# Kernel tuning notes

Hardware: AMD Instinct MI355X
Metric: run time of the kernel (lower is better)

Reference implementation:

```python
import jax, jax.numpy as jnp
import numpy as np

HID = 8
PRED_LEN = 12
SCALE = 4.4


def lstm_cell(x, h, c, Wih, Whh, bih, bhh):
    # torch.nn.LSTMCell gate order: i, f, g, o
    gates = x @ Wih.T + h @ Whh.T + (bih + bhh)  # (B, 4*HID)
    i, f, g, o = jnp.split(gates, 4, axis=-1)
    i = jax.nn.sigmoid(i)
    f = jax.nn.sigmoid(f)
    g = jnp.tanh(g)
    o = jax.nn.sigmoid(o)
    c_new = f * c + i * g
    h_new = o * jnp.tanh(c_new)
    return h_new, c_new


def setup_inputs() -> dict:
    key = jax.random.key(0)
    ks = jax.random.split(key, 12)
    B = 1048576
    obs_traj = jax.random.normal(ks[0], (8, B, 2), dtype=jnp.float32)
    h0 = jax.random.normal(ks[1], (B, HID), dtype=jnp.float32)
    c0 = jax.random.normal(ks[2], (B, HID), dtype=jnp.float32)
    s = 0.1
    Wih_t = jax.random.normal(ks[3], (4 * HID, 2), dtype=jnp.float32) * s
    Whh_t = jax.random.normal(ks[4], (4 * HID, HID), dtype=jnp.float32) * s
    bih_t = jax.random.normal(ks[5], (4 * HID,), dtype=jnp.float32) * s
    bhh_t = jax.random.normal(ks[6], (4 * HID,), dtype=jnp.float32) * s
    Wih_p = jax.random.normal(ks[7], (4 * HID, 2), dtype=jnp.float32) * s
    Whh_p = jax.random.normal(ks[8], (4 * HID, HID), dtype=jnp.float32) * s
    bih_p = jax.random.normal(ks[9], (4 * HID,), dtype=jnp.float32) * s
    bhh_p = jax.random.normal(ks[10], (4 * HID,), dtype=jnp.float32) * s
    Wp = jax.random.normal(ks[11], (2, HID), dtype=jnp.float32) * s
    bp = jnp.zeros((2,), dtype=jnp.float32)
    return {"obs_traj": obs_traj, "h0": h0, "c0": c0,
            "Wih_t": Wih_t, "Whh_t": Whh_t, "bih_t": bih_t, "bhh_t": bhh_t,
            "Wih_p": Wih_p, "Whh_p": Whh_p, "bih_p": bih_p, "bhh_p": bhh_p,
            "Wp": Wp, "bp": bp}


def reference(obs_traj, h0, c0, Wih_t, Whh_t, bih_t, bhh_t,
              Wih_p, Whh_p, bih_p, bhh_p, Wp, bp):
    B = obs_traj.shape[1]

    # --- encoder: scan over obs_len steps ---
    def enc_step(carry, x_t):
        h, c = carry
        x = jax.nn.relu(x_t)  # F.relu(input_t)
        h, c = lstm_cell(x, h, c, Wih_t, Whh_t, bih_t, bhh_t)
        return (h, c), None

    (h_enc, _), _ = jax.lax.scan(enc_step, (h0, c0), obs_traj)

    h_dec = h_enc
    c_dec = jnp.zeros_like(h_enc)
    out0 = jnp.zeros((B, 2), dtype=obs_traj.dtype)

    def dec_step(carry, _):
        h, c, out = carry
        x = jax.lax.stop_gradient(out)  # output.detach()
        h, c = lstm_cell(x, h, c, Wih_p, Whh_p, bih_p, bhh_p)
        out = jnp.tanh(h @ Wp.T + bp) * SCALE
        return (h, c, out), out

    _, pred_traj = jax.lax.scan(dec_step, (h_dec, c_dec, out0), None, length=PRED_LEN)
    return pred_traj  # (PRED_LEN, B, 2)
```

## Files before the change

kernel.cpp:

```cpp
#include <hip/hip_runtime.h>

#define HID 8
#define OBS_LEN 8
#define PRED_LEN 12
#define SCALE 4.4f
#define BLOCK 256
#define ELEMS_PER_BLOCK 128

#define LOG2E 1.44269504f
#define ECLAMP 16.0f

typedef __attribute__((ext_vector_type(8)))  _Float16 half8;
typedef __attribute__((ext_vector_type(2)))  _Float16 half2v;
typedef __attribute__((ext_vector_type(16))) float    f32x16;
typedef __attribute__((ext_vector_type(2)))  float    v2f;

union H8 { half8 v; half2v p[4]; };
struct AB { half8 hi, lo; };
struct H2 { _Float16 hi, lo; };

__device__ __forceinline__ v2f splat(float v) { v2f r; r.x = v; r.y = v; return r; }

__device__ __forceinline__ v2f vfma(v2f a, v2f b, v2f c) {
    return __builtin_elementwise_fma(a, b, c);
}

__device__ __forceinline__ v2f exp2v(v2f a) {
    v2f r;
    r.x = __builtin_amdgcn_exp2f(a.x);
    r.y = __builtin_amdgcn_exp2f(a.y);
    return r;
}

__device__ __forceinline__ half2v pkrtz(float a, float b) {
    return __builtin_bit_cast(half2v, __builtin_amdgcn_cvt_pkrtz(a, b));
}

__device__ __forceinline__ H2 split1(float v) {
    H2 r;
    r.hi = (_Float16)v;
    r.lo = (_Float16)(v - (float)r.hi);
    return r;
}

__device__ __forceinline__ void split_pair_v(v2f ab, half2v& hi, half2v& lo) {
    hi = pkrtz(ab.x, ab.y);
    v2f hc; hc.x = (float)hi.x; hc.y = (float)hi.y;
    const v2f res = ab - hc;
    lo = pkrtz(res.x, res.y);
}

__device__ __forceinline__ void quad_inv(const v2f d[2], v2f inv[2]) {
    const v2f p2 = d[0] * d[1];
    const float r = __builtin_amdgcn_rcpf(p2.x * p2.y);
    const v2f t = splat(r) * p2;
    v2f ts; ts.x = t.y; ts.y = t.x;
    inv[0] = ts * d[1];
    inv[1] = ts * d[0];
}

__device__ __forceinline__ AB build_A(int m, int half_,
    const float* __restrict__ Wih, const float* __restrict__ Whh,
    const float* __restrict__ bih, const float* __restrict__ bhh)
{
    const float k = ((m >> 3) == 2) ? (-2.0f * LOG2E) : (-LOG2E);
    float w[8];
    if (half_ == 0) {
        w[0] = Wih[m * 2 + 0] * k;
        w[1] = Wih[m * 2 + 1] * k;
        w[2] = Whh[m * 8 + 0] * k;
        w[3] = Whh[m * 8 + 1] * k;
        w[4] = Whh[m * 8 + 2] * k;
        w[5] = Whh[m * 8 + 3] * k;
        w[6] = (bih[m] + bhh[m]) * k;
        w[7] = 0.0f;
    } else {
        w[0] = 0.0f;
        w[1] = 0.0f;
        w[2] = Whh[m * 8 + 4] * k;
        w[3] = Whh[m * 8 + 5] * k;
        w[4] = Whh[m * 8 + 6] * k;
        w[5] = Whh[m * 8 + 7] * k;
        w[6] = 0.0f;
        w[7] = 0.0f;
    }
    AB r;
#pragma unroll
    for (int i = 0; i < 8; ++i) {
        const H2 s = split1(w[i]);
        r.hi[i] = s.hi;
        r.lo[i] = s.lo;
    }
    return r;
}

__device__ __forceinline__ AB build_B(v2f x01, const v2f h[2]) {
    H8 hi, lo;
    split_pair_v(x01, hi.p[0], lo.p[0]);
    split_pair_v(h[0], hi.p[1], lo.p[1]);
    split_pair_v(h[1], hi.p[2], lo.p[2]);
    const half2v one0 = {(_Float16)1.0f, (_Float16)0.0f};
    const half2v zz   = {(_Float16)0.0f, (_Float16)0.0f};
    hi.p[3] = one0;
    lo.p[3] = zz;
    AB r; r.hi = hi.v; r.lo = lo.v;
    return r;
}

__device__ __forceinline__ void lstm_pointwise(const f32x16& acc, v2f c[2], v2f h[2]) {
    const v2f vone = splat(1.0f);
    v2f num1[2], den1[2], uo[2];
#pragma unroll
    for (int p = 0; p < 2; ++p) {
        v2f ai, af, ag, ao;
        ai.x = acc[2 * p + 0];  ai.y = acc[2 * p + 1];
        af.x = acc[4 + 2 * p];  af.y = acc[5 + 2 * p];
        ag.x = acc[8 + 2 * p];  ag.y = acc[9 + 2 * p];
        ao.x = acc[12 + 2 * p]; ao.y = acc[13 + 2 * p];
        const v2f ei = exp2v(ai);
        const v2f ef = exp2v(af);
        const v2f eg = exp2v(ag);
        const v2f eo = exp2v(ao);
        const v2f uf = ef + vone;
        const v2f vg = eg + vone;
        const v2f tg = vone - eg;
        const v2f uiv = vfma(ei, vg, vg);
        num1[p] = vfma(tg, uf, c[p] * uiv);
        den1[p] = uf * uiv;
        uo[p] = eo + vone;
    }
    v2f inv1[2];
    quad_inv(den1, inv1);

    v2f den2[2], ecs[2];
#pragma unroll
    for (int p = 0; p < 2; ++p) {
        const v2f cn = num1[p] * inv1[p];
        c[p] = cn;
        const v2f s0 = cn * splat(-2.0f * LOG2E);
        v2f s; s.x = fminf(s0.x, ECLAMP); s.y = fminf(s0.y, ECLAMP);
        const v2f ec = exp2v(s);
        den2[p] = vfma(ec, uo[p], uo[p]);
        ecs[p] = ec;
    }
    v2f inv2[2];
    quad_inv(den2, inv2);
    h[0] = vfma(-ecs[0], inv2[0], inv2[0]);
    h[1] = vfma(-ecs[1], inv2[1], inv2[1]);
}

__device__ __forceinline__ void lstm_mfma_step(const AB& A, const AB& B, const f32x16& Z,
                                               v2f c[2], v2f h[2]) {
    f32x16 acc = __builtin_amdgcn_mfma_f32_32x32x16_f16(A.hi, B.hi, Z, 0, 0, 0);
    acc = __builtin_amdgcn_mfma_f32_32x32x16_f16(A.hi, B.lo, acc, 0, 0, 0);
    acc = __builtin_amdgcn_mfma_f32_32x32x16_f16(A.lo, B.hi, acc, 0, 0, 0);
    lstm_pointwise(acc, c, h);
}

__global__ __launch_bounds__(BLOCK) void MYLSTM_88201448390683_kernel(
    const float* __restrict__ obs,
    const float* __restrict__ h0,
    const float* __restrict__ c0,
    const float* __restrict__ Wih_t, const float* __restrict__ Whh_t,
    const float* __restrict__ bih_t, const float* __restrict__ bhh_t,
    const float* __restrict__ Wih_p, const float* __restrict__ Whh_p,
    const float* __restrict__ bih_p, const float* __restrict__ bhh_p,
    const float* __restrict__ Wp,
    const float* __restrict__ bp,
    float* __restrict__ out,
    int B)
{
    const int lane = threadIdx.x & 63;
    const int wid  = threadIdx.x >> 6;
    const int e    = lane & 31;
    const int half = lane >> 5;

    int eg = blockIdx.x * ELEMS_PER_BLOCK + wid * 32 + e;
    const bool ok = eg < B;
    if (!ok) eg = 0;

    const f32x16 kZero = {};

    v2f h[2], c[2];
    {
        const float4 hv = *reinterpret_cast<const float4*>(h0 + (size_t)eg * HID + half * 4);
        const float4 cv = *reinterpret_cast<const float4*>(c0 + (size_t)eg * HID + half * 4);
        h[0].x = hv.x; h[0].y = hv.y; h[1].x = hv.z; h[1].y = hv.w;
        c[0].x = cv.x; c[0].y = cv.y; c[1].x = cv.z; c[1].y = cv.w;
    }

    {
        const AB Aenc = build_A(e, half, Wih_t, Whh_t, bih_t, bhh_t);
        const float* op = obs + (size_t)eg * 2;
        const size_t ostride = (size_t)B * 2;
#pragma unroll 1
        for (int t = 0; t < OBS_LEN; ++t) {
            const v2f xv = *reinterpret_cast<const v2f*>(op);
            op += ostride;
            v2f xr; xr.x = fmaxf(xv.x, 0.0f); xr.y = fmaxf(xv.y, 0.0f);
            const AB Bv = build_B(xr, h);
            lstm_mfma_step(Aenc, Bv, kZero, c, h);
        }
    }

    const AB Adec = build_A(e, half, Wih_p, Whh_p, bih_p, bhh_p);
    c[0] = splat(0.0f);
    c[1] = splat(0.0f);

    v2f wa[2], wb[2];
    wa[0].x = Wp[4 * half + 0];       wa[0].y = Wp[4 * half + 1];
    wa[1].x = Wp[4 * half + 2];       wa[1].y = Wp[4 * half + 3];
    wb[0].x = Wp[HID + 4 * half + 0]; wb[0].y = Wp[HID + 4 * half + 1];
    wb[1].x = Wp[HID + 4 * half + 2]; wb[1].y = Wp[HID + 4 * half + 3];
    v2f b0v, b1v;
    b0v.x = half ? 0.0f : bp[0]; b0v.y = 0.0f;
    b1v.x = half ? 0.0f : bp[1]; b1v.y = 0.0f;

    v2f x01 = splat(0.0f);
#pragma unroll 1
    for (int t = 0; t < PRED_LEN; ++t) {
        const AB Bv = build_B(x01, h);
        lstm_mfma_step(Adec, Bv, kZero, c, h);
        const v2f q0 = vfma(wa[1], h[1], vfma(wa[0], h[0], b0v));
        const v2f q1 = vfma(wb[1], h[1], vfma(wb[0], h[0], b1v));
        float a0 = q0.x + q0.y;
        float a1 = q1.x + q1.y;
        a0 += __shfl_xor(a0, 32);
        a1 += __shfl_xor(a1, 32);
        v2f av; av.x = a0; av.y = a1;
        const v2f ev = exp2v(av * splat(-2.0f * LOG2E));
        const v2f den = ev + splat(1.0f);
        const float r = __builtin_amdgcn_rcpf(den.x * den.y);
        v2f ds; ds.x = den.y; ds.y = den.x;
        const v2f invv = splat(r) * ds;
        const v2f tn = splat(1.0f) - ev;
        x01 = (tn * invv) * splat(SCALE);
        if (!half && ok) {
            *reinterpret_cast<float2*>(out + ((size_t)t * B + eg) * 2) = make_float2(x01.x, x01.y);
        }
    }
}

extern "C" void kernel_launch(void* const* d_in, const int* in_sizes, int n_in,
                              void* d_out, int out_size, void* d_ws, size_t ws_size,
                              hipStream_t stream) {
    const float* obs   = (const float*)d_in[0];
    const float* h0    = (const float*)d_in[1];
    const float* c0    = (const float*)d_in[2];
    const float* Wih_t = (const float*)d_in[3];
    const float* Whh_t = (const float*)d_in[4];
    const float* bih_t = (const float*)d_in[5];
    const float* bhh_t = (const float*)d_in[6];
    const float* Wih_p = (const float*)d_in[7];
    const float* Whh_p = (const float*)d_in[8];
    const float* bih_p = (const float*)d_in[9];
    const float* bhh_p = (const float*)d_in[10];
    const float* Wp    = (const float*)d_in[11];
    const float* bp    = (const float*)d_in[12];
    float* out = (float*)d_out;

    const int B = in_sizes[1] / HID;
    const int grid = (B + ELEMS_PER_BLOCK - 1) / ELEMS_PER_BLOCK;

    hipLaunchKernelGGL(MYLSTM_88201448390683_kernel, dim3(grid), dim3(BLOCK), 0, stream,
                       obs, h0, c0,
                       Wih_t, Whh_t, bih_t, bhh_t,
                       Wih_p, Whh_p, bih_p, bhh_p,
                       Wp, bp, out, B);
}
```

Baseline: 334.3 us.

## Drop one MFMA per LSTM step by packing x's lo-split into the spare half's K slots

The input x's hi/lo split is folded into the single B operand: half 0 carries the hi part and half 1 the residual lo part, with Wih weights duplicated into both halves of A. h is rounded to fp16 with round-to-nearest and its lo correction term is dropped, so each step uses two MFMAs instead of three. The exception is the first encoder step, where h0 still gets a full lo pass. A small fma fusion is also applied to the output tanh. This cuts matrix-core work per step, at the cost of hidden-state precision (h keeps only about fp16 accuracy), which could affect the accuracy tolerance.

```diff
diff --git a/kernel.cpp b/kernel.cpp
--- a/kernel.cpp
+++ b/kernel.cpp
@@ -36,18 +36,15 @@
     return __builtin_bit_cast(half2v, __builtin_amdgcn_cvt_pkrtz(a, b));
 }
 
+__device__ __forceinline__ half2v rne2(v2f v) {
+    half2v r; r.x = (_Float16)v.x; r.y = (_Float16)v.y; return r;
+}
+
 __device__ __forceinline__ H2 split1(float v) {
     H2 r;
     r.hi = (_Float16)v;
     r.lo = (_Float16)(v - (float)r.hi);
     return r;
-}
-
-__device__ __forceinline__ void split_pair_v(v2f ab, half2v& hi, half2v& lo) {
-    hi = pkrtz(ab.x, ab.y);
-    v2f hc; hc.x = (float)hi.x; hc.y = (float)hi.y;
-    const v2f res = ab - hc;
-    lo = pkrtz(res.x, res.y);
 }
 
 __device__ __forceinline__ void quad_inv(const v2f d[2], v2f inv[2]) {
@@ -65,25 +62,22 @@
 {
     const float k = ((m >> 3) == 2) ? (-2.0f * LOG2E) : (-LOG2E);
     float w[8];
+    w[0] = Wih[m * 2 + 0] * k;
+    w[1] = Wih[m * 2 + 1] * k;
     if (half_ == 0) {
-        w[0] = Wih[m * 2 + 0] * k;
-        w[1] = Wih[m * 2 + 1] * k;
         w[2] = Whh[m * 8 + 0] * k;
         w[3] = Whh[m * 8 + 1] * k;
         w[4] = Whh[m * 8 + 2] * k;
         w[5] = Whh[m * 8 + 3] * k;
         w[6] = (bih[m] + bhh[m]) * k;
-        w[7] = 0.0f;
     } else {
-        w[0] = 0.0f;
-        w[1] = 0.0f;
         w[2] = Whh[m * 8 + 4] * k;
         w[3] = Whh[m * 8 + 5] * k;
         w[4] = Whh[m * 8 + 6] * k;
         w[5] = Whh[m * 8 + 7] * k;
         w[6] = 0.0f;
-        w[7] = 0.0f;
-    }
+    }
+    w[7] = 0.0f;
     AB r;
 #pragma unroll
     for (int i = 0; i < 8; ++i) {
@@ -94,17 +88,31 @@
     return r;
 }
 
-__device__ __forceinline__ AB build_B(v2f x01, const v2f h[2]) {
-    H8 hi, lo;
-    split_pair_v(x01, hi.p[0], lo.p[0]);
-    split_pair_v(h[0], hi.p[1], lo.p[1]);
-    split_pair_v(h[1], hi.p[2], lo.p[2]);
+__device__ __forceinline__ half8 build_B_hi(v2f x01, const v2f h[2], bool half1) {
+    H8 hi;
+    const half2v xh = pkrtz(x01.x, x01.y);
+    v2f hc; hc.x = (float)xh.x; hc.y = (float)xh.y;
+    const v2f res = x01 - hc;
+    const half2v xl = pkrtz(res.x, res.y);
+    hi.p[0] = half1 ? xl : xh;
+    hi.p[1] = rne2(h[0]);
+    hi.p[2] = rne2(h[1]);
     const half2v one0 = {(_Float16)1.0f, (_Float16)0.0f};
-    const half2v zz   = {(_Float16)0.0f, (_Float16)0.0f};
     hi.p[3] = one0;
+    return hi.v;
+}
+
+__device__ __forceinline__ half8 build_B_lo_h(const v2f h[2], half8 bh) {
+    H8 hb; hb.v = bh;
+    H8 lo;
+    v2f r0; r0.x = h[0].x - (float)hb.p[1].x; r0.y = h[0].y - (float)hb.p[1].y;
+    v2f r1; r1.x = h[1].x - (float)hb.p[2].x; r1.y = h[1].y - (float)hb.p[2].y;
+    const half2v zz = {(_Float16)0.0f, (_Float16)0.0f};
+    lo.p[0] = zz;
+    lo.p[1] = pkrtz(r0.x, r0.y);
+    lo.p[2] = pkrtz(r1.x, r1.y);
     lo.p[3] = zz;
-    AB r; r.hi = hi.v; r.lo = lo.v;
-    return r;
+    return lo.v;
 }
 
 __device__ __forceinline__ void lstm_pointwise(const f32x16& acc, v2f c[2], v2f h[2]) {
@@ -149,11 +157,10 @@
     h[1] = vfma(-ecs[1], inv2[1], inv2[1]);
 }
 
-__device__ __forceinline__ void lstm_mfma_step(const AB& A, const AB& B, const f32x16& Z,
-                                               v2f c[2], v2f h[2]) {
-    f32x16 acc = __builtin_amdgcn_mfma_f32_32x32x16_f16(A.hi, B.hi, Z, 0, 0, 0);
-    acc = __builtin_amdgcn_mfma_f32_32x32x16_f16(A.hi, B.lo, acc, 0, 0, 0);
-    acc = __builtin_amdgcn_mfma_f32_32x32x16_f16(A.lo, B.hi, acc, 0, 0, 0);
+__device__ __forceinline__ void lstm_step2(const AB& A, const half8& Bh, const f32x16& Z,
+                                           v2f c[2], v2f h[2]) {
+    f32x16 acc = __builtin_amdgcn_mfma_f32_32x32x16_f16(A.hi, Bh, Z, 0, 0, 0);
+    acc = __builtin_amdgcn_mfma_f32_32x32x16_f16(A.lo, Bh, acc, 0, 0, 0);
     lstm_pointwise(acc, c, h);
 }
 
@@ -174,6 +181,7 @@
     const int wid  = threadIdx.x >> 6;
     const int e    = lane & 31;
     const int half = lane >> 5;
+    const bool half1 = half != 0;
 
     int eg = blockIdx.x * ELEMS_PER_BLOCK + wid * 32 + e;
     const bool ok = eg < B;
@@ -193,13 +201,24 @@
         const AB Aenc = build_A(e, half, Wih_t, Whh_t, bih_t, bhh_t);
         const float* op = obs + (size_t)eg * 2;
         const size_t ostride = (size_t)B * 2;
-#pragma unroll 1
-        for (int t = 0; t < OBS_LEN; ++t) {
+        {
             const v2f xv = *reinterpret_cast<const v2f*>(op);
             op += ostride;
             v2f xr; xr.x = fmaxf(xv.x, 0.0f); xr.y = fmaxf(xv.y, 0.0f);
-            const AB Bv = build_B(xr, h);
-            lstm_mfma_step(Aenc, Bv, kZero, c, h);
+            const half8 Bh = build_B_hi(xr, h, half1);
+            const half8 Bl = build_B_lo_h(h, Bh);
+            f32x16 acc = __builtin_amdgcn_mfma_f32_32x32x16_f16(Aenc.hi, Bh, kZero, 0, 0, 0);
+            acc = __builtin_amdgcn_mfma_f32_32x32x16_f16(Aenc.lo, Bh, acc, 0, 0, 0);
+            acc = __builtin_amdgcn_mfma_f32_32x32x16_f16(Aenc.hi, Bl, acc, 0, 0, 0);
+            lstm_pointwise(acc, c, h);
+        }
+#pragma unroll 1
+        for (int t = 1; t < OBS_LEN; ++t) {
+            const v2f xv = *reinterpret_cast<const v2f*>(op);
+            op += ostride;
+            v2f xr; xr.x = fmaxf(xv.x, 0.0f); xr.y = fmaxf(xv.y, 0.0f);
+            const half8 Bh = build_B_hi(xr, h, half1);
+            lstm_step2(Aenc, Bh, kZero, c, h);
         }
     }
 
@@ -219,8 +238,8 @@
     v2f x01 = splat(0.0f);
 #pragma unroll 1
     for (int t = 0; t < PRED_LEN; ++t) {
-        const AB Bv = build_B(x01, h);
-        lstm_mfma_step(Adec, Bv, kZero, c, h);
+        const half8 Bv = build_B_hi(x01, h, half1);
+        lstm_step2(Adec, Bv, kZero, c, h);
         const v2f q0 = vfma(wa[1], h[1], vfma(wa[0], h[0], b0v));
         const v2f q1 = vfma(wb[1], h[1], vfma(wb[0], h[0], b1v));
         float a0 = q0.x + q0.y;
@@ -232,9 +251,8 @@
         const v2f den = ev + splat(1.0f);
         const float r = __builtin_amdgcn_rcpf(den.x * den.y);
         v2f ds; ds.x = den.y; ds.y = den.x;
-        const v2f invv = splat(r) * ds;
-        const v2f tn = splat(1.0f) - ev;
-        x01 = (tn * invv) * splat(SCALE);
+        const v2f q = (splat(r) * ds) * splat(SCALE);
+        x01 = vfma(-ev, q, q);
         if (!half && ok) {
             *reinterpret_cast<float2*>(out + ((size_t)t * B + eg) * 2) = make_float2(x01.x, x01.y);
         }
```

Result: no change. 329.6 us (-1.4%).
